# Performance work log

Measured on AMD Instinct MI355X. Metric: run time of the kernel, lower is better.

The kernel has to match this reference:

```python
import jax, jax.numpy as jnp
import numpy as np

N, E, D = 20000, 160000, 128   # nodes, edges, d_model
GH, HC = 4, 128                # TransformerConv heads, per-head channels (= out_channels)
MH = 4                         # temporal MHA heads
MC = D // MH                   # temporal MHA per-head dim
EPS = 1e-5


def layer_norm(x, g, b):
    mu = x.mean(-1, keepdims=True)
    var = ((x - mu) ** 2).mean(-1, keepdims=True)
    return (x - mu) * jax.lax.rsqrt(var + EPS) * g + b


def forward(x, temporal_encoding, gq_w, gq_b, gk_w, gk_b, gv_w, gv_b, gs_w, gs_b,
            mha_wq, mha_bq, mha_wk, mha_bk, mha_wv, mha_bv, mha_wo, mha_bo,
            ffn_w1, ffn_b1, ffn_w2, ffn_b2,
            ln1_g, ln1_b, ln2_g, ln2_b, ln3_g, ln3_b, edge_index):
    src, dst = edge_index[0], edge_index[1]
    n = x.shape[0]
    # --- TransformerConv(in=D, out=D, heads=GH, concat=False, root_weight=True) ---
    q = (x @ gq_w.T + gq_b).reshape(n, GH, HC)
    k = (x @ gk_w.T + gk_b).reshape(n, GH, HC)
    v = (x @ gv_w.T + gv_b).reshape(n, GH, HC)
    # per-edge attention logits: <q_i, k_j> / sqrt(out_channels), message j->i
    alpha = (q[dst] * k[src]).sum(-1) / jnp.sqrt(jnp.asarray(HC, x.dtype))  # [E, GH]
    # numerically-stable segment softmax over incoming edges of each dst node
    m = jax.ops.segment_max(alpha, dst, num_segments=n)                     # [N, GH]
    ex = jnp.exp(alpha - m[dst])
    den = jax.ops.segment_sum(ex, dst, num_segments=n)
    w = ex / den[dst]                                                       # [E, GH]
    agg = jax.ops.segment_sum(w[..., None] * v[src], dst, num_segments=n)  # [N, GH, HC]
    graph_out = agg.mean(1) + (x @ gs_w.T + gs_b)  # concat=False -> head mean; + root skip lin
    x1 = layer_norm(x + graph_out, ln1_g, ln1_b)   # dropout is identity at eval
    # --- temporal MHA: per-node query (len 1) attends to its temporal encoding (kv len 1) ---
    tq = (x1 @ mha_wq.T + mha_bq).reshape(n, MH, MC)
    tk = (temporal_encoding @ mha_wk.T + mha_bk).reshape(n, MH, MC)
    tv = (temporal_encoding @ mha_wv.T + mha_bv).reshape(n, MH, MC)
    scores = (tq * tk).sum(-1, keepdims=True) / jnp.sqrt(jnp.asarray(MC, x.dtype))  # [N, MH, 1]
    attn = jax.nn.softmax(scores, axis=-1)  # exactly ones (single kv position); kept for fidelity
    temp_out = (attn * tv).reshape(n, D) @ mha_wo.T + mha_bo
    x2 = layer_norm(x1 + temp_out, ln2_g, ln2_b)
    # --- FFN ---
    h = jax.nn.relu(x2 @ ffn_w1.T + ffn_b1)
    ffn_out = h @ ffn_w2.T + ffn_b2
    return layer_norm(x2 + ffn_out, ln3_g, ln3_b)


def setup_inputs() -> dict:
    ks = jax.random.split(jax.random.key(0), 16)
    s = 0.05
    def p(i, shape):
        return jax.random.normal(ks[i], shape, jnp.float32) * s
    z = lambda *sh: jnp.zeros(sh, jnp.float32)
    o = lambda *sh: jnp.ones(sh, jnp.float32)
    return {
        "x": p(0, (N, D)),
        "temporal_encoding": p(1, (N, D)),
        "gq_w": p(2, (GH * HC, D)), "gq_b": z(GH * HC),
        "gk_w": p(3, (GH * HC, D)), "gk_b": z(GH * HC),
        "gv_w": p(4, (GH * HC, D)), "gv_b": z(GH * HC),
        "gs_w": p(5, (D, D)), "gs_b": z(D),
        "mha_wq": p(6, (D, D)), "mha_bq": z(D),
        "mha_wk": p(7, (D, D)), "mha_bk": z(D),
        "mha_wv": p(8, (D, D)), "mha_bv": z(D),
        "mha_wo": p(9, (D, D)), "mha_bo": z(D),
        "ffn_w1": p(10, (4 * D, D)), "ffn_b1": z(4 * D),
        "ffn_w2": p(11, (D, 4 * D)), "ffn_b2": z(D),
        "ln1_g": o(D), "ln1_b": z(D),
        "ln2_g": o(D), "ln2_b": z(D),
        "ln3_g": o(D), "ln3_b": z(D),
        "edge_index": jax.random.randint(ks[12], (2, E), 0, N, jnp.int32),
    }


def reference(x, temporal_encoding, gq_w, gq_b, gk_w, gk_b, gv_w, gv_b, gs_w, gs_b,
              mha_wq, mha_bq, mha_wk, mha_bk, mha_wv, mha_bv, mha_wo, mha_bo,
              ffn_w1, ffn_b1, ffn_w2, ffn_b2,
              ln1_g, ln1_b, ln2_g, ln2_b, ln3_g, ln3_b, edge_index):
    return forward(x, temporal_encoding, gq_w, gq_b, gk_w, gk_b, gv_w, gv_b, gs_w, gs_b,
                   mha_wq, mha_bq, mha_wk, mha_bk, mha_wv, mha_bv, mha_wo, mha_bo,
                   ffn_w1, ffn_b1, ffn_w2, ffn_b2,
                   ln1_g, ln1_b, ln2_g, ln2_b, ln3_g, ln3_b, edge_index)
```

## Files before the change

### kernel.cpp

```cpp
#include <hip/hip_runtime.h>

#define NN 20000
#define EE 160000
#define DD 128
#define GHC 512
#define INV_SQRT_HC 0.08838834764831845f

typedef __attribute__((ext_vector_type(8))) short short8;
typedef __attribute__((ext_vector_type(4))) short short4v;
typedef __attribute__((ext_vector_type(4))) float float4v;
typedef __attribute__((ext_vector_type(2))) float float2v;
typedef __attribute__((ext_vector_type(4))) unsigned uint4v;
typedef __attribute__((ext_vector_type(2))) unsigned uint2v;

__device__ inline float bf2f(unsigned short u) {
    union { unsigned u; float f; } x; x.u = ((unsigned)u) << 16; return x.f;
}
__device__ inline unsigned short f2bf(float f) {
    union { float f; unsigned u; } x; x.f = f;
    unsigned u = x.u;
    unsigned r = (u + 0x7fffu + ((u >> 16) & 1u)) >> 16;
    return (unsigned short)r;
}
__device__ inline unsigned cvt_pk_bf16(float a, float b) {
    unsigned d;
    asm("v_cvt_pk_bf16_f32 %0, %1, %2" : "=v"(d) : "v"(a), "v"(b));
    return d;
}

__device__ inline void stage16(const short8* gsrc, short8* ldst) {
    __builtin_amdgcn_global_load_lds(
        (const __attribute__((address_space(1))) void*)gsrc,
        (__attribute__((address_space(3))) void*)ldst, 16, 0, 0);
}

#if defined(__has_builtin)
#if __has_builtin(__builtin_amdgcn_cvt_pk_f32_fp8) && __has_builtin(__builtin_amdgcn_cvt_pk_fp8_f32)
#define HW_FP8 1
#endif
#endif
#ifndef HW_FP8
#define HW_FP8 0
#endif

#if !HW_FP8
__device__ inline unsigned char sw_enc_fp8(float f) {
    if (!(f == f)) return 0x7f;
    unsigned s = (f < 0.f) ? 0x80u : 0u;
    float a = fabsf(f);
    if (a >= 448.f) return (unsigned char)(s | 0x7e);
    if (a < 5.96046448e-8f) return (unsigned char)s;
    int e; frexpf(a, &e);
    int E = e - 1;
    if (E < -6) E = -6;
    float q = ldexpf(rintf(ldexpf(a, 3 - E)), E - 3);
    if (q == 0.f) return (unsigned char)s;
    union { float f; unsigned u; } x; x.f = q;
    int qe = (int)((x.u >> 23) & 0xff) - 127;
    if (qe < -6) {
        unsigned mant = (unsigned)rintf(ldexpf(q, 9));
        return (unsigned char)(s | mant);
    }
    unsigned mant = (x.u >> 20) & 7;
    int ebits = qe + 7;
    if (ebits > 15) { ebits = 15; mant = 6; }
    return (unsigned char)(s | ((unsigned)ebits << 3) | mant);
}
__device__ inline float sw_dec_fp8(unsigned char u) {
    unsigned s = u >> 7, e = (u >> 3) & 15, m = u & 7;
    float v = e ? ldexpf((float)(8 + m), (int)e - 10) : ldexpf((float)m, -9);
    return s ? -v : v;
}
#endif

__device__ inline unsigned fp8_enc4(float a, float b, float c, float d) {
#if HW_FP8
    int r = __builtin_amdgcn_cvt_pk_fp8_f32(a, b, 0, false);
    r = __builtin_amdgcn_cvt_pk_fp8_f32(c, d, r, true);
    return (unsigned)r;
#else
    return (unsigned)sw_enc_fp8(a) | ((unsigned)sw_enc_fp8(b) << 8)
         | ((unsigned)sw_enc_fp8(c) << 16) | ((unsigned)sw_enc_fp8(d) << 24);
#endif
}
__device__ inline float2v fp8_dec2_lo(unsigned w) {
#if HW_FP8
    return __builtin_amdgcn_cvt_pk_f32_fp8((int)w, false);
#else
    float2v r;
    r[0] = sw_dec_fp8((unsigned char)(w & 0xff));
    r[1] = sw_dec_fp8((unsigned char)((w >> 8) & 0xff));
    return r;
#endif
}
__device__ inline float2v fp8_dec2_hi(unsigned w) {
#if HW_FP8
    return __builtin_amdgcn_cvt_pk_f32_fp8((int)w, true);
#else
    float2v r;
    r[0] = sw_dec_fp8((unsigned char)((w >> 16) & 0xff));
    r[1] = sw_dec_fp8((unsigned char)(w >> 24));
    return r;
#endif
}

struct WPack { const void* in[18]; };
__device__ __constant__ const int WSZ[18] = {
    65536, 65536, 65536, 512, 512, 512,
    16384, 128, 65536, 512, 65536, 128,
    128, 128, 128, 128, 128, 128 };

__global__ void prep_kernel(const float* __restrict__ x, const float* __restrict__ te,
                            unsigned short* __restrict__ xcout, WPack p,
                            unsigned short* __restrict__ wcout,
                            const float* __restrict__ wv, const float* __restrict__ bv,
                            const float* __restrict__ wo, const float* __restrict__ bo,
                            unsigned short* __restrict__ wcomb,
                            unsigned short* __restrict__ bcomb,
                            const int* __restrict__ e_dst, int* __restrict__ counts)
{
    const int b = blockIdx.x;
    const int tid = threadIdx.x;
    if (b < 1024) {
        const long n4half = (long)NN * DD / 4;
        short4v* out4 = reinterpret_cast<short4v*>(xcout);
        long i = (long)b * 256 + tid;
        const long stride = 1024L * 256;
        const long tot = 2 * n4half;
        for (; i < tot; i += stride) {
            const float4v* src = (i < n4half)
                ? reinterpret_cast<const float4v*>(x)
                : reinterpret_cast<const float4v*>(te) - n4half;
            float4v v = src[i];
            short4v o;
            o[0] = (short)f2bf(v[0]); o[1] = (short)f2bf(v[1]);
            o[2] = (short)f2bf(v[2]); o[3] = (short)f2bf(v[3]);
            out4[i] = o;
        }
    } else if (b < 1600) {
        const int seg = (b - 1024) >> 5;
        const int rep = (b - 1024) & 31;
        int off = 0;
#pragma unroll
        for (int s = 0; s < 18; ++s) if (s < seg) off += WSZ[s];
        const int n = WSZ[seg];
        const float* q = (const float*)p.in[seg];
        for (int i = rep * 256 + tid; i < n; i += 32 * 256)
            wcout[off + i] = f2bf(q[i]);
    } else if (b < 1664) {
        int e = (b - 1600) * 256 + tid;
        int i = e >> 7, kk = e & 127;
        float s = 0.f;
        for (int j = 0; j < 128; ++j)
            s += wo[i * 128 + j] * wv[j * 128 + kk];
        wcomb[e] = f2bf(s);
        if (b == 1600 && tid < 128) {
            float t = 0.f;
            for (int j = 0; j < 128; ++j) t += wo[tid * 128 + j] * bv[j];
            bcomb[tid] = f2bf(t + bo[tid]);
        }
    } else {
        int e = (b - 1664) * 256 + tid;
        if (e < EE) {
            int d = e_dst[e];
            if (d >= 0 && d < NN) atomicAdd(&counts[d], 1);
        }
    }
}

__global__ __launch_bounds__(256) void gemm3_kernel(
    const unsigned short* __restrict__ A, const unsigned short* __restrict__ W,
    const unsigned short* __restrict__ bias, unsigned short* __restrict__ out,
    unsigned char* __restrict__ kvout, int M, int Nout, int split, int relu,
    int nxg, int ncol)
{
    __shared__ short8 wslab[2048];
    __shared__ __attribute__((aligned(16))) unsigned stile4[4][16][32];
    const int tid  = threadIdx.x;
    const int lane = tid & 63;
    const int wid  = tid >> 6;
    const int quad = lane >> 4;
    const int l15  = lane & 15;

    const int nb  = nxg * ncol;
    const int qq  = nb >> 3, rm = nb & 7;
    const int xcd = blockIdx.x & 7, slot = blockIdx.x >> 3;
    const int c   = (xcd < rm) ? xcd * (qq + 1) + slot
                               : rm * (qq + 1) + (xcd - rm) * qq + slot;
    const int xg = c / ncol;
    const int yg = c - xg * ncol;
    const int colbase0 = yg * 128;
    const int rowg = xg * 256;

    const bool isfp8 = (colbase0 >= split);
    const int kvcol = colbase0 - split;
    const int which = isfp8 ? (kvcol >> 9) : 0;
    const int head  = isfp8 ? ((kvcol & 511) >> 7) : 0;

    const short8* A8 = reinterpret_cast<const short8*>(A);
    const short8* W8 = reinterpret_cast<const short8*>(W);

    short8 a4[4];
    {
        int arow = rowg + wid * 16 + l15;
        if (arow >= M) arow = M - 1;
#pragma unroll
        for (int i = 0; i < 4; ++i) a4[i] = A8[(size_t)arow * 16 + i * 4 + quad];
    }

#pragma unroll
    for (int rep = 0; rep < 8; ++rep) {
        const int fi  = (rep * 4 + wid) & 3;
        const int ft  = rep & 3;
        const int ftt = rep >> 2;
        const int wrow = colbase0 + ftt * 64 + 16 * ft + l15;
        stage16(&W8[(size_t)wrow * 16 + fi * 4 + quad], &wslab[rep * 256 + wid * 64]);
    }

    short4v bs4[2][4];
#pragma unroll
    for (int tt = 0; tt < 2; ++tt)
#pragma unroll
        for (int t = 0; t < 4; ++t)
            bs4[tt][t] = *reinterpret_cast<const short4v*>(
                &bias[colbase0 + tt * 64 + 16 * t + quad * 4]);

    __syncthreads();

    unsigned* fpd = &stile4[wid][0][0];

#pragma unroll
    for (int tg = 0; tg < 4; ++tg) {
        const int rowbase = rowg + tg * 64 + wid * 16;

        short8 a4n[4];
        if (tg < 3) {
            int arow = rowbase + 64 + l15;
            if (arow >= M) arow = M - 1;
#pragma unroll
            for (int i = 0; i < 4; ++i) a4n[i] = A8[(size_t)arow * 16 + i * 4 + quad];
        }

#pragma unroll
        for (int tt = 0; tt < 2; ++tt) {
            float4v acc[4];
#pragma unroll
            for (int t = 0; t < 4; ++t) acc[t] = (float4v){0.f, 0.f, 0.f, 0.f};

#pragma unroll
            for (int i = 0; i < 4; ++i) {
#pragma unroll
                for (int t = 0; t < 4; ++t) {
                    short8 wb = wslab[((tt * 4 + t) * 4 + i) * 64 + lane];
                    acc[t] = __builtin_amdgcn_mfma_f32_16x16x32_bf16(wb, a4[i], acc[t], 0, 0, 0);
                }
            }

            if (!isfp8) {
#pragma unroll
                for (int t = 0; t < 4; ++t) {
                    float v0 = acc[t][0] + bf2f((unsigned short)bs4[tt][t][0]);
                    float v1 = acc[t][1] + bf2f((unsigned short)bs4[tt][t][1]);
                    float v2 = acc[t][2] + bf2f((unsigned short)bs4[tt][t][2]);
                    float v3 = acc[t][3] + bf2f((unsigned short)bs4[tt][t][3]);
                    if (relu) {
                        v0 = fmaxf(v0, 0.f); v1 = fmaxf(v1, 0.f);
                        v2 = fmaxf(v2, 0.f); v3 = fmaxf(v3, 0.f);
                    }
                    uint2v d = { cvt_pk_bf16(v0, v1), cvt_pk_bf16(v2, v3) };
                    const int dc = (8 * t + quad * 2) ^ ((l15 & 7) << 2);
                    *reinterpret_cast<uint2v*>(&stile4[wid][l15][dc]) = d;
                }
                const int rr0 = lane >> 3;
                const int cd  = (lane & 7) * 4;
#pragma unroll
                for (int it = 0; it < 2; ++it) {
                    int rw = rr0 + it * 8;
                    int grow = rowbase + rw;
                    if (grow < M) {
                        const int cs = cd ^ ((rw & 7) << 2);
                        uint4v v = *reinterpret_cast<const uint4v*>(&stile4[wid][rw][cs]);
                        *reinterpret_cast<uint4v*>(&out[(size_t)grow * Nout + colbase0 + tt * 64 + cd * 2]) = v;
                    }
                }
            } else {
#pragma unroll
                for (int t = 0; t < 4; ++t) {
                    float v0 = (acc[t][0] + bf2f((unsigned short)bs4[tt][t][0])) * 256.f;
                    float v1 = (acc[t][1] + bf2f((unsigned short)bs4[tt][t][1])) * 256.f;
                    float v2 = (acc[t][2] + bf2f((unsigned short)bs4[tt][t][2])) * 256.f;
                    float v3 = (acc[t][3] + bf2f((unsigned short)bs4[tt][t][3])) * 256.f;
                    const int dc = (tt * 16 + 4 * t + quad) ^ ((l15 & 7) << 2);
                    fpd[l15 * 32 + dc] = fp8_enc4(v0, v1, v2, v3);
                }
            }
        }

        if (isfp8) {
#pragma unroll
            for (int it = 0; it < 2; ++it) {
                int u = lane + it * 64;
                int row = u >> 3;
                int part = u & 7;
                int grow = rowbase + row;
                if (grow < M) {
                    const int db = row * 32 + ((part * 4) ^ ((row & 7) << 2));
                    uint4v v = *reinterpret_cast<const uint4v*>(&fpd[db]);
                    size_t ro = (size_t)grow * 1024 + (size_t)which * 512
                              + (size_t)head * 128 + (size_t)part * 16;
                    *reinterpret_cast<uint4v*>(kvout + ro) = v;
                }
            }
        }

        if (tg < 3) {
#pragma unroll
            for (int i = 0; i < 4; ++i) a4[i] = a4n[i];
        }
    }
}

__global__ __launch_bounds__(256) void gemm_ln2_kernel(
    const unsigned short* __restrict__ A, const unsigned short* __restrict__ W,
    const unsigned short* __restrict__ bias,
    const float* __restrict__ residf, const float* __restrict__ c,
    const unsigned short* __restrict__ g, const unsigned short* __restrict__ beta,
    float* __restrict__ outf, unsigned short* __restrict__ outb, int M, int K)
{
    __shared__ short8 wslab[2048];
    const int tid  = threadIdx.x;
    const int lane = tid & 63;
    const int wid  = tid >> 6;
    const int quad = lane >> 4;
    const int l15  = lane & 15;
    const int rowbase = blockIdx.x * 64 + wid * 16;

    const int grow = rowbase + l15;
    const int gr = (grow < M) ? grow : M - 1;

    const short8* A8 = reinterpret_cast<const short8*>(A);
    const short8* W8 = reinterpret_cast<const short8*>(W);
    const int k8 = K >> 3;
    const int kchunks = K >> 7;

    float4v acc[2][4];
#pragma unroll
    for (int tt = 0; tt < 2; ++tt)
#pragma unroll
        for (int t = 0; t < 4; ++t) acc[tt][t] = (float4v){0.f, 0.f, 0.f, 0.f};

    for (int cc = 0; cc < kchunks; ++cc) {
        if (cc > 0) __syncthreads();
#pragma unroll
        for (int rep = 0; rep < 8; ++rep) {
            const int fi  = (rep * 4 + wid) & 3;
            const int ft  = rep & 3;
            const int ftt = rep >> 2;
            const int wrow = ftt * 64 + 16 * ft + l15;
            stage16(&W8[(size_t)wrow * k8 + cc * 16 + fi * 4 + quad],
                    &wslab[rep * 256 + wid * 64]);
        }
        short8 a4[4];
#pragma unroll
        for (int i = 0; i < 4; ++i) a4[i] = A8[(size_t)gr * k8 + cc * 16 + i * 4 + quad];
        __syncthreads();
#pragma unroll
        for (int tt = 0; tt < 2; ++tt)
#pragma unroll
            for (int i = 0; i < 4; ++i)
#pragma unroll
                for (int t = 0; t < 4; ++t) {
                    short8 wb = wslab[((tt * 4 + t) * 4 + i) * 64 + lane];
                    acc[tt][t] = __builtin_amdgcn_mfma_f32_16x16x32_bf16(wb, a4[i], acc[tt][t], 0, 0, 0);
                }
    }

    float v[32];
#pragma unroll
    for (int tt = 0; tt < 2; ++tt)
#pragma unroll
        for (int t = 0; t < 4; ++t) {
            const int n0 = tt * 64 + 16 * t + quad * 4;
            short4v bs = *reinterpret_cast<const short4v*>(&bias[n0]);
            float4v rv = *reinterpret_cast<const float4v*>(&residf[(size_t)gr * 128 + n0]);
#pragma unroll
            for (int r = 0; r < 4; ++r)
                v[(tt * 4 + t) * 4 + r] = acc[tt][t][r]
                    + bf2f((unsigned short)bs[r]) + rv[r];
        }
    if (c) {
#pragma unroll
        for (int tt = 0; tt < 2; ++tt)
#pragma unroll
            for (int t = 0; t < 4; ++t) {
                const int n0 = tt * 64 + 16 * t + quad * 4;
                float4v cv = *reinterpret_cast<const float4v*>(&c[(size_t)gr * 128 + n0]);
#pragma unroll
                for (int r = 0; r < 4; ++r) v[(tt * 4 + t) * 4 + r] += cv[r];
            }
    }
    float s = 0.f, sq = 0.f;
#pragma unroll
    for (int i = 0; i < 32; ++i) { s += v[i]; sq += v[i] * v[i]; }
    s  += __shfl_xor(s, 16, 64);  s  += __shfl_xor(s, 32, 64);
    sq += __shfl_xor(sq, 16, 64); sq += __shfl_xor(sq, 32, 64);
    float mu  = s * (1.f / 128.f);
    float var = sq * (1.f / 128.f) - mu * mu;
    float rs  = rsqrtf(fmaxf(var, 0.f) + 1e-5f);

    if (grow < M) {
#pragma unroll
        for (int tt = 0; tt < 2; ++tt)
#pragma unroll
            for (int t = 0; t < 4; ++t) {
                const int n0 = tt * 64 + 16 * t + quad * 4;
                short4v gg = *reinterpret_cast<const short4v*>(&g[n0]);
                short4v bb = *reinterpret_cast<const short4v*>(&beta[n0]);
                float4v ov;
#pragma unroll
                for (int r = 0; r < 4; ++r)
                    ov[r] = (v[(tt * 4 + t) * 4 + r] - mu) * rs
                            * bf2f((unsigned short)gg[r]) + bf2f((unsigned short)bb[r]);
                *reinterpret_cast<float4v*>(&outf[(size_t)grow * 128 + n0]) = ov;
                if (outb) {
                    uint2v d = { cvt_pk_bf16(ov[0], ov[1]), cvt_pk_bf16(ov[2], ov[3]) };
                    *reinterpret_cast<uint2v*>(&outb[(size_t)grow * 128 + n0]) = d;
                }
            }
    }
}

__global__ __launch_bounds__(256) void gemm_ln12_kernel(
    const unsigned short* __restrict__ A1, const unsigned short* __restrict__ W1,
    const unsigned short* __restrict__ b1,
    const float* __restrict__ rx, const float* __restrict__ ragg,
    const unsigned short* __restrict__ g1, const unsigned short* __restrict__ be1,
    const unsigned short* __restrict__ A2, const unsigned short* __restrict__ W2,
    const unsigned short* __restrict__ b2,
    const unsigned short* __restrict__ g2, const unsigned short* __restrict__ be2,
    float* __restrict__ outf, unsigned short* __restrict__ outb, int M)
{
    __shared__ short8 wslab[2048];
    const int tid  = threadIdx.x;
    const int lane = tid & 63;
    const int wid  = tid >> 6;
    const int quad = lane >> 4;
    const int l15  = lane & 15;
    const int rowbase = blockIdx.x * 64 + wid * 16;

    const int grow = rowbase + l15;
    const int gr = (grow < M) ? grow : M - 1;

    const short8* A81 = reinterpret_cast<const short8*>(A1);
    const short8* A82 = reinterpret_cast<const short8*>(A2);
    const short8* W81 = reinterpret_cast<const short8*>(W1);
    const short8* W82 = reinterpret_cast<const short8*>(W2);

#pragma unroll
    for (int rep = 0; rep < 8; ++rep) {
        const int fi  = (rep * 4 + wid) & 3;
        const int ft  = rep & 3;
        const int ftt = rep >> 2;
        const int wrow = ftt * 64 + 16 * ft + l15;
        stage16(&W81[(size_t)wrow * 16 + fi * 4 + quad], &wslab[rep * 256 + wid * 64]);
    }
    short8 a4[4];
#pragma unroll
    for (int i = 0; i < 4; ++i) a4[i] = A81[(size_t)gr * 16 + i * 4 + quad];
    __syncthreads();

    float4v acc1[2][4];
#pragma unroll
    for (int tt = 0; tt < 2; ++tt)
#pragma unroll
        for (int t = 0; t < 4; ++t) acc1[tt][t] = (float4v){0.f, 0.f, 0.f, 0.f};
#pragma unroll
    for (int tt = 0; tt < 2; ++tt)
#pragma unroll
        for (int i = 0; i < 4; ++i)
#pragma unroll
            for (int t = 0; t < 4; ++t) {
                short8 wb = wslab[((tt * 4 + t) * 4 + i) * 64 + lane];
                acc1[tt][t] = __builtin_amdgcn_mfma_f32_16x16x32_bf16(wb, a4[i], acc1[tt][t], 0, 0, 0);
            }
    __syncthreads();

#pragma unroll
    for (int rep = 0; rep < 8; ++rep) {
        const int fi  = (rep * 4 + wid) & 3;
        const int ft  = rep & 3;
        const int ftt = rep >> 2;
        const int wrow = ftt * 64 + 16 * ft + l15;
        stage16(&W82[(size_t)wrow * 16 + fi * 4 + quad], &wslab[rep * 256 + wid * 64]);
    }
    short8 a42[4];
#pragma unroll
    for (int i = 0; i < 4; ++i) a42[i] = A82[(size_t)gr * 16 + i * 4 + quad];

    float x1[32];
    {
        float v[32];
#pragma unroll
        for (int tt = 0; tt < 2; ++tt)
#pragma unroll
            for (int t = 0; t < 4; ++t) {
                const int n0 = tt * 64 + 16 * t + quad * 4;
                short4v bs = *reinterpret_cast<const short4v*>(&b1[n0]);
                float4v rv = *reinterpret_cast<const float4v*>(&rx[(size_t)gr * 128 + n0]);
                float4v cv = *reinterpret_cast<const float4v*>(&ragg[(size_t)gr * 128 + n0]);
#pragma unroll
                for (int r = 0; r < 4; ++r)
                    v[(tt * 4 + t) * 4 + r] = acc1[tt][t][r]
                        + bf2f((unsigned short)bs[r]) + rv[r] + cv[r];
            }
        float s = 0.f, sq = 0.f;
#pragma unroll
        for (int i = 0; i < 32; ++i) { s += v[i]; sq += v[i] * v[i]; }
        s  += __shfl_xor(s, 16, 64);  s  += __shfl_xor(s, 32, 64);
        sq += __shfl_xor(sq, 16, 64); sq += __shfl_xor(sq, 32, 64);
        float mu  = s * (1.f / 128.f);
        float var = sq * (1.f / 128.f) - mu * mu;
        float rs  = rsqrtf(fmaxf(var, 0.f) + 1e-5f);
#pragma unroll
        for (int tt = 0; tt < 2; ++tt)
#pragma unroll
            for (int t = 0; t < 4; ++t) {
                const int n0 = tt * 64 + 16 * t + quad * 4;
                short4v gg = *reinterpret_cast<const short4v*>(&g1[n0]);
                short4v bb = *reinterpret_cast<const short4v*>(&be1[n0]);
#pragma unroll
                for (int r = 0; r < 4; ++r)
                    x1[(tt * 4 + t) * 4 + r] = (v[(tt * 4 + t) * 4 + r] - mu) * rs
                        * bf2f((unsigned short)gg[r]) + bf2f((unsigned short)bb[r]);
            }
    }

    __syncthreads();

    float4v acc2[2][4];
#pragma unroll
    for (int tt = 0; tt < 2; ++tt)
#pragma unroll
        for (int t = 0; t < 4; ++t) acc2[tt][t] = (float4v){0.f, 0.f, 0.f, 0.f};
#pragma unroll
    for (int tt = 0; tt < 2; ++tt)
#pragma unroll
        for (int i = 0; i < 4; ++i)
#pragma unroll
            for (int t = 0; t < 4; ++t) {
                short8 wb = wslab[((tt * 4 + t) * 4 + i) * 64 + lane];
                acc2[tt][t] = __builtin_amdgcn_mfma_f32_16x16x32_bf16(wb, a42[i], acc2[tt][t], 0, 0, 0);
            }

    float v[32];
#pragma unroll
    for (int tt = 0; tt < 2; ++tt)
#pragma unroll
        for (int t = 0; t < 4; ++t) {
            const int n0 = tt * 64 + 16 * t + quad * 4;
            short4v bs = *reinterpret_cast<const short4v*>(&b2[n0]);
#pragma unroll
            for (int r = 0; r < 4; ++r)
                v[(tt * 4 + t) * 4 + r] = acc2[tt][t][r]
                    + bf2f((unsigned short)bs[r]) + x1[(tt * 4 + t) * 4 + r];
        }
    float s = 0.f, sq = 0.f;
#pragma unroll
    for (int i = 0; i < 32; ++i) { s += v[i]; sq += v[i] * v[i]; }
    s  += __shfl_xor(s, 16, 64);  s  += __shfl_xor(s, 32, 64);
    sq += __shfl_xor(sq, 16, 64); sq += __shfl_xor(sq, 32, 64);
    float mu  = s * (1.f / 128.f);
    float var = sq * (1.f / 128.f) - mu * mu;
    float rs  = rsqrtf(fmaxf(var, 0.f) + 1e-5f);

    if (grow < M) {
#pragma unroll
        for (int tt = 0; tt < 2; ++tt)
#pragma unroll
            for (int t = 0; t < 4; ++t) {
                const int n0 = tt * 64 + 16 * t + quad * 4;
                short4v gg = *reinterpret_cast<const short4v*>(&g2[n0]);
                short4v bb = *reinterpret_cast<const short4v*>(&be2[n0]);
                float4v ov;
#pragma unroll
                for (int r = 0; r < 4; ++r)
                    ov[r] = (v[(tt * 4 + t) * 4 + r] - mu) * rs
                            * bf2f((unsigned short)gg[r]) + bf2f((unsigned short)bb[r]);
                *reinterpret_cast<float4v*>(&outf[(size_t)grow * 128 + n0]) = ov;
                uint2v d = { cvt_pk_bf16(ov[0], ov[1]), cvt_pk_bf16(ov[2], ov[3]) };
                *reinterpret_cast<uint2v*>(&outb[(size_t)grow * 128 + n0]) = d;
            }
    }
}

__global__ __launch_bounds__(1024) void scan_kernel(
    const int* __restrict__ counts, int* __restrict__ offsets, int* __restrict__ pos, int n)
{
    __shared__ int wsum[16];
    __shared__ int carry_s;
    const int tid = threadIdx.x;
    const int wid = tid >> 6, lane = tid & 63;
    int vals[20];
#pragma unroll
    for (int cI = 0; cI < 20; ++cI) {
        int i = cI * 1024 + tid;
        vals[cI] = (i < n) ? counts[i] : 0;
    }
    if (tid == 0) carry_s = 0;
    __syncthreads();
#pragma unroll
    for (int cI = 0; cI < 20; ++cI) {
        int i = cI * 1024 + tid;
        int val = vals[cI];
        int x = val;
#pragma unroll
        for (int off = 1; off < 64; off <<= 1) {
            int t = __shfl_up(x, off, 64);
            if (lane >= off) x += t;
        }
        if (lane == 63) wsum[wid] = x;
        __syncthreads();
        if (wid == 0 && lane < 16) {
            int s = wsum[lane];
#pragma unroll
            for (int off = 1; off < 16; off <<= 1) {
                int t = __shfl_up(s, off, 64);
                if (lane >= off) s += t;
            }
            wsum[lane] = s;
        }
        __syncthreads();
        int prefix = (wid > 0 ? wsum[wid - 1] : 0) + carry_s;
        int ex = prefix + x - val;
        if (i < n) { offsets[i] = ex; pos[i] = ex; }
        __syncthreads();
        if (tid == 0) carry_s += wsum[15];
        __syncthreads();
    }
    if (tid == 0) offsets[n] = carry_s;
}

__global__ void scatter_kernel(const int* __restrict__ src, const int* __restrict__ dst,
                               int* __restrict__ pos, int* __restrict__ sorted_src, int E)
{
    int e = blockIdx.x * 256 + threadIdx.x;
    if (e < E) {
        int d = dst[e];
        if (d >= 0 && d < NN) {
            int p = atomicAdd(&pos[d], 1);
            if (p >= 0 && p < E) sorted_src[p] = src[e];
        }
    }
}

__device__ inline void agg_edge(const uint2v& kk, const uint2v& vv,
                                const float* qf, float* acc, float& ssum)
{
    float2v k01 = fp8_dec2_lo(kk[0]);
    float2v k23 = fp8_dec2_hi(kk[0]);
    float2v k45 = fp8_dec2_lo(kk[1]);
    float2v k67 = fp8_dec2_hi(kk[1]);
    float dot = qf[0] * k01[0] + qf[1] * k01[1] + qf[2] * k23[0] + qf[3] * k23[1]
              + qf[4] * k45[0] + qf[5] * k45[1] + qf[6] * k67[0] + qf[7] * k67[1];
    dot += __shfl_xor(dot, 1, 64);
    dot += __shfl_xor(dot, 2, 64);
    dot += __shfl_xor(dot, 4, 64);
    dot += __shfl_xor(dot, 8, 64);
    float pp = __expf(dot);
    ssum += pp;
    float2v v01 = fp8_dec2_lo(vv[0]);
    float2v v23 = fp8_dec2_hi(vv[0]);
    float2v v45 = fp8_dec2_lo(vv[1]);
    float2v v67 = fp8_dec2_hi(vv[1]);
    acc[0] += pp * v01[0]; acc[1] += pp * v01[1];
    acc[2] += pp * v23[0]; acc[3] += pp * v23[1];
    acc[4] += pp * v45[0]; acc[5] += pp * v45[1];
    acc[6] += pp * v67[0]; acc[7] += pp * v67[1];
}

__global__ __launch_bounds__(256) void agg_kernel(
    const unsigned short* __restrict__ q, const unsigned char* __restrict__ kvb,
    const int* __restrict__ offsets, const int* __restrict__ srcs,
    float* __restrict__ aggb)
{
    __shared__ float sacc[4][64][9];
    __shared__ float sssum[4][64];
    const int tid  = threadIdx.x;
    const int wid  = tid >> 6;
    const int lane = tid & 63;
    const int node = blockIdx.x * 2 + (wid >> 1);
    const int half = wid & 1;

    const short8* q8 = reinterpret_cast<const short8*>(q);
    const int fidx = (lane >> 4) * 16 + (lane & 15);
    const int koff = fidx * 8;

    short8 qv = q8[(size_t)node * 64 + fidx];
    float qf[8];
#pragma unroll
    for (int i = 0; i < 8; ++i)
        qf[i] = bf2f((unsigned short)qv[i]) * (INV_SQRT_HC / 256.f);

    int beg = offsets[node], end = offsets[node + 1];
    if (beg < 0) beg = 0;
    if (end > EE) end = EE;
    float ssum = 0.f;
    float acc[8];
#pragma unroll
    for (int i = 0; i < 8; ++i) acc[i] = 0.f;

    const int start = beg + half;
    int nce = (end > start) ? ((end - start + 1) >> 1) : 0;
    int ncap = (nce > 64) ? 64 : nce;

    int sv = 0;
    if (lane < ncap) {
        int s = srcs[start + 2 * lane];
        if (s < 0) s = 0;
        if (s >= NN) s = NN - 1;
        sv = s;
    }
    for (int base = 0; base < ncap; base += 4) {
        const int rem = ncap - base;
        uint2v k0{}, v0{}, k1{}, v1{}, k2{}, v2{}, k3{}, v3{};
        {
            int s = __shfl(sv, base, 64);
            const unsigned char* p = kvb + (size_t)s * 1024 + koff;
            k0 = *reinterpret_cast<const uint2v*>(p);
            v0 = *reinterpret_cast<const uint2v*>(p + 512);
        }
        if (rem > 1) {
            int s = __shfl(sv, base + 1, 64);
            const unsigned char* p = kvb + (size_t)s * 1024 + koff;
            k1 = *reinterpret_cast<const uint2v*>(p);
            v1 = *reinterpret_cast<const uint2v*>(p + 512);
        }
        if (rem > 2) {
            int s = __shfl(sv, base + 2, 64);
            const unsigned char* p = kvb + (size_t)s * 1024 + koff;
            k2 = *reinterpret_cast<const uint2v*>(p);
            v2 = *reinterpret_cast<const uint2v*>(p + 512);
        }
        if (rem > 3) {
            int s = __shfl(sv, base + 3, 64);
            const unsigned char* p = kvb + (size_t)s * 1024 + koff;
            k3 = *reinterpret_cast<const uint2v*>(p);
            v3 = *reinterpret_cast<const uint2v*>(p + 512);
        }
        agg_edge(k0, v0, qf, acc, ssum);
        if (rem > 1) agg_edge(k1, v1, qf, acc, ssum);
        if (rem > 2) agg_edge(k2, v2, qf, acc, ssum);
        if (rem > 3) agg_edge(k3, v3, qf, acc, ssum);
    }
    for (int j = start + 128; j < end; j += 2) {
        int s = srcs[j];
        if (s < 0) s = 0;
        if (s >= NN) s = NN - 1;
        uint2v kc = *reinterpret_cast<const uint2v*>(kvb + (size_t)s * 1024 + koff);
        uint2v vc = *reinterpret_cast<const uint2v*>(kvb + (size_t)s * 1024 + 512 + koff);
        agg_edge(kc, vc, qf, acc, ssum);
    }

#pragma unroll
    for (int i = 0; i < 8; ++i) sacc[wid][lane][i] = acc[i];
    sssum[wid][lane] = ssum;
    __syncthreads();
    if (half == 0) {
#pragma unroll
        for (int i = 0; i < 8; ++i) acc[i] += sacc[wid ^ 1][lane][i];
        ssum += sssum[wid ^ 1][lane];

        float inv = (ssum > 0.f) ? 1.f / (256.f * ssum) : 0.f;
#pragma unroll
        for (int i = 0; i < 8; ++i) acc[i] *= inv;
#pragma unroll
        for (int i = 0; i < 8; ++i) {
            acc[i] += __shfl_xor(acc[i], 16, 64);
            acc[i] += __shfl_xor(acc[i], 32, 64);
            acc[i] *= 0.25f;
        }
        if (lane < 16) {
            float4v* o = reinterpret_cast<float4v*>(aggb + (size_t)node * 128 + lane * 8);
            o[0] = (float4v){acc[0], acc[1], acc[2], acc[3]};
            o[1] = (float4v){acc[4], acc[5], acc[6], acc[7]};
        }
    }
}

extern "C" void kernel_launch(void* const* d_in, const int* in_sizes, int n_in,
                              void* d_out, int out_size, void* d_ws, size_t ws_size,
                              hipStream_t stream)
{
    const int* edge_index = (const int*)d_in[28];
    const int* e_src = edge_index;
    const int* e_dst = edge_index + EE;

    if (n_in < 29 || in_sizes[0] != NN * DD || in_sizes[28] != 2 * EE || out_size != NN * DD)
        return;

    const size_t SZ_OFF  = (size_t)(NN + 16) * 4;
    const size_t SZ_CNT  = (size_t)NN * 4;
    const size_t SZ_SS   = (size_t)EE * 4;
    const size_t SZ_SM   = (size_t)NN * DD * 2;
    const size_t SZ_F32  = (size_t)NN * DD * 4;
    const size_t SZ_Q    = (size_t)NN * 512 * 2;
    const size_t SZ_KV   = (size_t)NN * 1024;
    const size_t SZ_HB   = (size_t)NN * GHC * 2;
    const size_t WC_ELE  = 347136;
    const size_t SZ_WC   = WC_ELE * 2;
    const size_t SZ_WCB  = 16384 * 2 + 256;
    const size_t REQUIRED = SZ_OFF + 2 * SZ_CNT + SZ_SS + 2 * SZ_SM + SZ_WC + SZ_WCB
                          + SZ_Q + SZ_KV + 3 * SZ_F32 + SZ_SM + SZ_HB;

    if (ws_size < REQUIRED) return;

    char* w = (char*)d_ws;
    int* offsets = (int*)w;        w += SZ_OFF;
    int* counts  = (int*)w;        w += SZ_CNT;
    int* pos     = (int*)w;        w += SZ_CNT;
    int* sorted_src = (int*)w;     w += SZ_SS;
    unsigned short* xc   = (unsigned short*)w; w += SZ_SM;
    unsigned short* tec  = (unsigned short*)w; w += SZ_SM;
    unsigned short* wc   = (unsigned short*)w; w += SZ_WC;
    unsigned short* wcomb = (unsigned short*)w; w += 16384 * 2;
    unsigned short* bcomb = (unsigned short*)w; w += 256;
    unsigned short* qb   = (unsigned short*)w; w += SZ_Q;
    unsigned char*  kvb  = (unsigned char*)w;  w += SZ_KV;
    float*          aggb = (float*)w;          w += SZ_F32;
    float*          x1f  = (float*)w;          w += SZ_F32;
    float*          x2f  = (float*)w;          w += SZ_F32;
    unsigned short* x2b  = (unsigned short*)w; w += SZ_SM;
    unsigned short* hbuf = (unsigned short*)w; w += SZ_HB;
    (void)x1f;

    unsigned short* cw = wc;
    unsigned short* qkv_w = cw; cw += 3 * 65536;
    unsigned short* qkv_b = cw; cw += 3 * 512;
    unsigned short* gs_w  = cw; cw += 16384;  unsigned short* gs_b  = cw; cw += 128;
    unsigned short* ffn_w1 = cw; cw += 65536; unsigned short* ffn_b1 = cw; cw += 512;
    unsigned short* ffn_w2 = cw; cw += 65536; unsigned short* ffn_b2 = cw; cw += 128;
    unsigned short* ln1_g = cw; cw += 128;    unsigned short* ln1_b = cw; cw += 128;
    unsigned short* ln2_g = cw; cw += 128;    unsigned short* ln2_b = cw; cw += 128;
    unsigned short* ln3_g = cw; cw += 128;    unsigned short* ln3_b = cw; cw += 128;

    const int EB = (EE + 255) / 256;
    const dim3 blk(256);
    const int MB = (NN + 63) / 64;
    const int MB2 = (NN + 255) / 256;

    WPack pack;
    const int live_idx[18] = {2,4,6, 3,5,7, 8,9, 18,19, 20,21, 22,23,24,25,26,27};
    for (int i = 0; i < 18; ++i) pack.in[i] = d_in[live_idx[i]];

    (void)hipMemsetAsync(counts, 0, SZ_CNT, stream);
    prep_kernel<<<1664 + EB, blk, 0, stream>>>((const float*)d_in[0], (const float*)d_in[1],
                                               xc, pack, wc,
                                               (const float*)d_in[14], (const float*)d_in[15],
                                               (const float*)d_in[16], (const float*)d_in[17],
                                               wcomb, bcomb, e_dst, counts);

    scan_kernel<<<1, 1024, 0, stream>>>(counts, offsets, pos, NN);
    scatter_kernel<<<EB, blk, 0, stream>>>(e_src, e_dst, pos, sorted_src, EE);

    gemm3_kernel<<<dim3(MB2 * 12), blk, 0, stream>>>(xc, qkv_w, qkv_b, qb, kvb,
                                                     NN, 512, 512, 0, MB2, 12);
    agg_kernel<<<NN / 2, blk, 0, stream>>>(qb, kvb, offsets, sorted_src, aggb);
    gemm_ln12_kernel<<<MB, blk, 0, stream>>>(xc, gs_w, gs_b,
                                             (const float*)d_in[0], aggb,
                                             ln1_g, ln1_b,
                                             tec, wcomb, bcomb,
                                             ln2_g, ln2_b, x2f, x2b, NN);
    gemm3_kernel<<<dim3(MB2 * 4), blk, 0, stream>>>(x2b, ffn_w1, ffn_b1, hbuf, nullptr,
                                                    NN, 512, 99999, 1, MB2, 4);
    gemm_ln2_kernel<<<MB, blk, 0, stream>>>(hbuf, ffn_w2, ffn_b2, x2f, nullptr,
                                            ln3_g, ln3_b, (float*)d_out, nullptr, NN, GHC);
}
```

Measured before the change: 259.8 us.

## Fuse LN1/LN2 GEMMs and full FFN into a single tail kernel

Merges the root-skip GEMM + LN1, temporal GEMM + LN2, FFN up-projection with ReLU, and FFN down-projection + LN3 into one kernel per 64-row tile. The 512-wide hidden activation is produced and consumed in 128-column chunks through a swizzled LDS tile, so it never goes to global memory. The x2 float/bf16 intermediates also stay on chip. This removes two launches and the global round trips of x2 and the hidden buffer. In exchange it adds LDS use, register pressure, more barriers, and only 313 blocks of parallelism for the FFN work instead of a wider grid.

```diff
diff --git a/kernel.cpp b/kernel.cpp
--- a/kernel.cpp
+++ b/kernel.cpp
@@ -320,50 +320,252 @@
     }
 }
 
-__global__ __launch_bounds__(256) void gemm_ln2_kernel(
-    const unsigned short* __restrict__ A, const unsigned short* __restrict__ W,
-    const unsigned short* __restrict__ bias,
-    const float* __restrict__ residf, const float* __restrict__ c,
-    const unsigned short* __restrict__ g, const unsigned short* __restrict__ beta,
-    float* __restrict__ outf, unsigned short* __restrict__ outb, int M, int K)
+__global__ __launch_bounds__(256) void tail_kernel(
+    const unsigned short* __restrict__ A1, const unsigned short* __restrict__ W1g,
+    const unsigned short* __restrict__ b1g,
+    const unsigned short* __restrict__ A2, const unsigned short* __restrict__ W2g,
+    const unsigned short* __restrict__ b2g,
+    const float* __restrict__ rx, const float* __restrict__ ragg,
+    const unsigned short* __restrict__ g1, const unsigned short* __restrict__ be1,
+    const unsigned short* __restrict__ g2, const unsigned short* __restrict__ be2,
+    const unsigned short* __restrict__ fw1, const unsigned short* __restrict__ fb1,
+    const unsigned short* __restrict__ fw2, const unsigned short* __restrict__ fb2,
+    const unsigned short* __restrict__ g3, const unsigned short* __restrict__ be3,
+    float* __restrict__ outf, int M)
 {
     __shared__ short8 wslab[2048];
+    __shared__ __attribute__((aligned(16))) unsigned short htile[64 * 128];
     const int tid  = threadIdx.x;
     const int lane = tid & 63;
     const int wid  = tid >> 6;
     const int quad = lane >> 4;
     const int l15  = lane & 15;
     const int rowbase = blockIdx.x * 64 + wid * 16;
-
     const int grow = rowbase + l15;
     const int gr = (grow < M) ? grow : M - 1;
-
-    const short8* A8 = reinterpret_cast<const short8*>(A);
-    const short8* W8 = reinterpret_cast<const short8*>(W);
-    const int k8 = K >> 3;
-    const int kchunks = K >> 7;
-
-    float4v acc[2][4];
+    const int hrow = wid * 16 + l15;
+    char* hb = reinterpret_cast<char*>(htile);
+
+    const short8* A81 = reinterpret_cast<const short8*>(A1);
+    const short8* A82 = reinterpret_cast<const short8*>(A2);
+    const short8* W81 = reinterpret_cast<const short8*>(W1g);
+    const short8* W82 = reinterpret_cast<const short8*>(W2g);
+    const short8* F18 = reinterpret_cast<const short8*>(fw1);
+    const short8* F28 = reinterpret_cast<const short8*>(fw2);
+
+#pragma unroll
+    for (int rep = 0; rep < 8; ++rep) {
+        const int fi  = (rep * 4 + wid) & 3;
+        const int ft  = rep & 3;
+        const int ftt = rep >> 2;
+        const int wrow = ftt * 64 + 16 * ft + l15;
+        stage16(&W81[(size_t)wrow * 16 + fi * 4 + quad], &wslab[rep * 256 + wid * 64]);
+    }
+    short8 a4[4];
+#pragma unroll
+    for (int i = 0; i < 4; ++i) a4[i] = A81[(size_t)gr * 16 + i * 4 + quad];
+    __syncthreads();
+
+    float4v acc1[2][4];
 #pragma unroll
     for (int tt = 0; tt < 2; ++tt)
 #pragma unroll
-        for (int t = 0; t < 4; ++t) acc[tt][t] = (float4v){0.f, 0.f, 0.f, 0.f};
-
-    for (int cc = 0; cc < kchunks; ++cc) {
-        if (cc > 0) __syncthreads();
+        for (int t = 0; t < 4; ++t) acc1[tt][t] = (float4v){0.f, 0.f, 0.f, 0.f};
+#pragma unroll
+    for (int tt = 0; tt < 2; ++tt)
+#pragma unroll
+        for (int i = 0; i < 4; ++i)
+#pragma unroll
+            for (int t = 0; t < 4; ++t) {
+                short8 wb = wslab[((tt * 4 + t) * 4 + i) * 64 + lane];
+                acc1[tt][t] = __builtin_amdgcn_mfma_f32_16x16x32_bf16(wb, a4[i], acc1[tt][t], 0, 0, 0);
+            }
+    __syncthreads();
+
+#pragma unroll
+    for (int rep = 0; rep < 8; ++rep) {
+        const int fi  = (rep * 4 + wid) & 3;
+        const int ft  = rep & 3;
+        const int ftt = rep >> 2;
+        const int wrow = ftt * 64 + 16 * ft + l15;
+        stage16(&W82[(size_t)wrow * 16 + fi * 4 + quad], &wslab[rep * 256 + wid * 64]);
+    }
+    short8 a42[4];
+#pragma unroll
+    for (int i = 0; i < 4; ++i) a42[i] = A82[(size_t)gr * 16 + i * 4 + quad];
+
+    float x1[32];
+    {
+        float v[32];
+#pragma unroll
+        for (int tt = 0; tt < 2; ++tt)
+#pragma unroll
+            for (int t = 0; t < 4; ++t) {
+                const int n0 = tt * 64 + 16 * t + quad * 4;
+                short4v bs = *reinterpret_cast<const short4v*>(&b1g[n0]);
+                float4v rv = *reinterpret_cast<const float4v*>(&rx[(size_t)gr * 128 + n0]);
+                float4v cv = *reinterpret_cast<const float4v*>(&ragg[(size_t)gr * 128 + n0]);
+#pragma unroll
+                for (int r = 0; r < 4; ++r)
+                    v[(tt * 4 + t) * 4 + r] = acc1[tt][t][r]
+                        + bf2f((unsigned short)bs[r]) + rv[r] + cv[r];
+            }
+        float s = 0.f, sq = 0.f;
+#pragma unroll
+        for (int i = 0; i < 32; ++i) { s += v[i]; sq += v[i] * v[i]; }
+        s  += __shfl_xor(s, 16, 64);  s  += __shfl_xor(s, 32, 64);
+        sq += __shfl_xor(sq, 16, 64); sq += __shfl_xor(sq, 32, 64);
+        float mu  = s * (1.f / 128.f);
+        float var = sq * (1.f / 128.f) - mu * mu;
+        float rs  = rsqrtf(fmaxf(var, 0.f) + 1e-5f);
+#pragma unroll
+        for (int tt = 0; tt < 2; ++tt)
+#pragma unroll
+            for (int t = 0; t < 4; ++t) {
+                const int n0 = tt * 64 + 16 * t + quad * 4;
+                short4v gg = *reinterpret_cast<const short4v*>(&g1[n0]);
+                short4v bb = *reinterpret_cast<const short4v*>(&be1[n0]);
+#pragma unroll
+                for (int r = 0; r < 4; ++r)
+                    x1[(tt * 4 + t) * 4 + r] = (v[(tt * 4 + t) * 4 + r] - mu) * rs
+                        * bf2f((unsigned short)gg[r]) + bf2f((unsigned short)bb[r]);
+            }
+    }
+
+    __syncthreads();
+
+    float4v acc2[2][4];
+#pragma unroll
+    for (int tt = 0; tt < 2; ++tt)
+#pragma unroll
+        for (int t = 0; t < 4; ++t) acc2[tt][t] = (float4v){0.f, 0.f, 0.f, 0.f};
+#pragma unroll
+    for (int tt = 0; tt < 2; ++tt)
+#pragma unroll
+        for (int i = 0; i < 4; ++i)
+#pragma unroll
+            for (int t = 0; t < 4; ++t) {
+                short8 wb = wslab[((tt * 4 + t) * 4 + i) * 64 + lane];
+                acc2[tt][t] = __builtin_amdgcn_mfma_f32_16x16x32_bf16(wb, a42[i], acc2[tt][t], 0, 0, 0);
+            }
+
+    float x2[32];
+    {
+        float v[32];
+#pragma unroll
+        for (int tt = 0; tt < 2; ++tt)
+#pragma unroll
+            for (int t = 0; t < 4; ++t) {
+                const int n0 = tt * 64 + 16 * t + quad * 4;
+                short4v bs = *reinterpret_cast<const short4v*>(&b2g[n0]);
+#pragma unroll
+                for (int r = 0; r < 4; ++r)
+                    v[(tt * 4 + t) * 4 + r] = acc2[tt][t][r]
+                        + bf2f((unsigned short)bs[r]) + x1[(tt * 4 + t) * 4 + r];
+            }
+        float s = 0.f, sq = 0.f;
+#pragma unroll
+        for (int i = 0; i < 32; ++i) { s += v[i]; sq += v[i] * v[i]; }
+        s  += __shfl_xor(s, 16, 64);  s  += __shfl_xor(s, 32, 64);
+        sq += __shfl_xor(sq, 16, 64); sq += __shfl_xor(sq, 32, 64);
+        float mu  = s * (1.f / 128.f);
+        float var = sq * (1.f / 128.f) - mu * mu;
+        float rs  = rsqrtf(fmaxf(var, 0.f) + 1e-5f);
+#pragma unroll
+        for (int tt = 0; tt < 2; ++tt)
+#pragma unroll
+            for (int t = 0; t < 4; ++t) {
+                const int n0 = tt * 64 + 16 * t + quad * 4;
+                short4v gg = *reinterpret_cast<const short4v*>(&g2[n0]);
+                short4v bb = *reinterpret_cast<const short4v*>(&be2[n0]);
+#pragma unroll
+                for (int r = 0; r < 4; ++r)
+                    x2[(tt * 4 + t) * 4 + r] = (v[(tt * 4 + t) * 4 + r] - mu) * rs
+                        * bf2f((unsigned short)gg[r]) + bf2f((unsigned short)bb[r]);
+            }
+    }
+
+#pragma unroll
+    for (int tt = 0; tt < 2; ++tt)
+#pragma unroll
+        for (int t = 0; t < 4; ++t) {
+            const int n0 = tt * 64 + 16 * t + quad * 4;
+            const int idx = (tt * 4 + t) * 4;
+            uint2v d = { cvt_pk_bf16(x2[idx], x2[idx + 1]),
+                         cvt_pk_bf16(x2[idx + 2], x2[idx + 3]) };
+            *reinterpret_cast<uint2v*>(
+                hb + ((hrow * 256 + n0 * 2) ^ ((hrow & 7) << 4))) = d;
+        }
+    short8 af[4];
+#pragma unroll
+    for (int i = 0; i < 4; ++i)
+        af[i] = *reinterpret_cast<const short8*>(
+            hb + ((hrow * 256 + (i * 32 + quad * 8) * 2) ^ ((hrow & 7) << 4)));
+
+    float4v accf[2][4];
+#pragma unroll
+    for (int tt = 0; tt < 2; ++tt)
+#pragma unroll
+        for (int t = 0; t < 4; ++t) accf[tt][t] = (float4v){0.f, 0.f, 0.f, 0.f};
+
+    for (int cc = 0; cc < 4; ++cc) {
+        __syncthreads();
+#pragma unroll
+        for (int rep = 0; rep < 8; ++rep) {
+            const int fi  = (rep * 4 + wid) & 3;
+            const int ft  = rep & 3;
+            const int ftt = rep >> 2;
+            const int wrow = cc * 128 + ftt * 64 + 16 * ft + l15;
+            stage16(&F18[(size_t)wrow * 16 + fi * 4 + quad], &wslab[rep * 256 + wid * 64]);
+        }
+        __syncthreads();
+
+        float4v au[2][4];
+#pragma unroll
+        for (int tt = 0; tt < 2; ++tt)
+#pragma unroll
+            for (int t = 0; t < 4; ++t) au[tt][t] = (float4v){0.f, 0.f, 0.f, 0.f};
+#pragma unroll
+        for (int tt = 0; tt < 2; ++tt)
+#pragma unroll
+            for (int i = 0; i < 4; ++i)
+#pragma unroll
+                for (int t = 0; t < 4; ++t) {
+                    short8 wb = wslab[((tt * 4 + t) * 4 + i) * 64 + lane];
+                    au[tt][t] = __builtin_amdgcn_mfma_f32_16x16x32_bf16(wb, af[i], au[tt][t], 0, 0, 0);
+                }
+#pragma unroll
+        for (int tt = 0; tt < 2; ++tt)
+#pragma unroll
+            for (int t = 0; t < 4; ++t) {
+                const int n0 = tt * 64 + 16 * t + quad * 4;
+                short4v bs = *reinterpret_cast<const short4v*>(&fb1[cc * 128 + n0]);
+                float v0 = fmaxf(au[tt][t][0] + bf2f((unsigned short)bs[0]), 0.f);
+                float v1 = fmaxf(au[tt][t][1] + bf2f((unsigned short)bs[1]), 0.f);
+                float v2 = fmaxf(au[tt][t][2] + bf2f((unsigned short)bs[2]), 0.f);
+                float v3 = fmaxf(au[tt][t][3] + bf2f((unsigned short)bs[3]), 0.f);
+                uint2v d = { cvt_pk_bf16(v0, v1), cvt_pk_bf16(v2, v3) };
+                *reinterpret_cast<uint2v*>(
+                    hb + ((hrow * 256 + n0 * 2) ^ ((hrow & 7) << 4))) = d;
+            }
+
+        __syncthreads();
 #pragma unroll
         for (int rep = 0; rep < 8; ++rep) {
             const int fi  = (rep * 4 + wid) & 3;
             const int ft  = rep & 3;
             const int ftt = rep >> 2;
             const int wrow = ftt * 64 + 16 * ft + l15;
-            stage16(&W8[(size_t)wrow * k8 + cc * 16 + fi * 4 + quad],
+            stage16(&F28[(size_t)wrow * 64 + cc * 16 + fi * 4 + quad],
                     &wslab[rep * 256 + wid * 64]);
         }
-        short8 a4[4];
-#pragma unroll
-        for (int i = 0; i < 4; ++i) a4[i] = A8[(size_t)gr * k8 + cc * 16 + i * 4 + quad];
         __syncthreads();
+
+        short8 h4[4];
+#pragma unroll
+        for (int i = 0; i < 4; ++i)
+            h4[i] = *reinterpret_cast<const short8*>(
+                hb + ((hrow * 256 + (i * 32 + quad * 8) * 2) ^ ((hrow & 7) << 4)));
 #pragma unroll
         for (int tt = 0; tt < 2; ++tt)
 #pragma unroll
@@ -371,7 +573,7 @@
 #pragma unroll
                 for (int t = 0; t < 4; ++t) {
                     short8 wb = wslab[((tt * 4 + t) * 4 + i) * 64 + lane];
-                    acc[tt][t] = __builtin_amdgcn_mfma_f32_16x16x32_bf16(wb, a4[i], acc[tt][t], 0, 0, 0);
+                    accf[tt][t] = __builtin_amdgcn_mfma_f32_16x16x32_bf16(wb, h4[i], accf[tt][t], 0, 0, 0);
                 }
     }
 
@@ -381,24 +583,12 @@
 #pragma unroll
         for (int t = 0; t < 4; ++t) {
             const int n0 = tt * 64 + 16 * t + quad * 4;
-            short4v bs = *reinterpret_cast<const short4v*>(&bias[n0]);
-            float4v rv = *reinterpret_cast<const float4v*>(&residf[(size_t)gr * 128 + n0]);
+            short4v bs = *reinterpret_cast<const short4v*>(&fb2[n0]);
 #pragma unroll
             for (int r = 0; r < 4; ++r)
-                v[(tt * 4 + t) * 4 + r] = acc[tt][t][r]
-                    + bf2f((unsigned short)bs[r]) + rv[r];
-        }
-    if (c) {
-#pragma unroll
-        for (int tt = 0; tt < 2; ++tt)
-#pragma unroll
-            for (int t = 0; t < 4; ++t) {
-                const int n0 = tt * 64 + 16 * t + quad * 4;
-                float4v cv = *reinterpret_cast<const float4v*>(&c[(size_t)gr * 128 + n0]);
-#pragma unroll
-                for (int r = 0; r < 4; ++r) v[(tt * 4 + t) * 4 + r] += cv[r];
-            }
-    }
+                v[(tt * 4 + t) * 4 + r] = accf[tt][t][r]
+                    + bf2f((unsigned short)bs[r]) + x2[(tt * 4 + t) * 4 + r];
+        }
     float s = 0.f, sq = 0.f;
 #pragma unroll
     for (int i = 0; i < 32; ++i) { s += v[i]; sq += v[i] * v[i]; }
@@ -414,181 +604,14 @@
 #pragma unroll
             for (int t = 0; t < 4; ++t) {
                 const int n0 = tt * 64 + 16 * t + quad * 4;
-                short4v gg = *reinterpret_cast<const short4v*>(&g[n0]);
-                short4v bb = *reinterpret_cast<const short4v*>(&beta[n0]);
+                short4v gg = *reinterpret_cast<const short4v*>(&g3[n0]);
+                short4v bb = *reinterpret_cast<const short4v*>(&be3[n0]);
                 float4v ov;
 #pragma unroll
                 for (int r = 0; r < 4; ++r)
                     ov[r] = (v[(tt * 4 + t) * 4 + r] - mu) * rs
                             * bf2f((unsigned short)gg[r]) + bf2f((unsigned short)bb[r]);
                 *reinterpret_cast<float4v*>(&outf[(size_t)grow * 128 + n0]) = ov;
-                if (outb) {
-                    uint2v d = { cvt_pk_bf16(ov[0], ov[1]), cvt_pk_bf16(ov[2], ov[3]) };
-                    *reinterpret_cast<uint2v*>(&outb[(size_t)grow * 128 + n0]) = d;
-                }
-            }
-    }
-}
-
-__global__ __launch_bounds__(256) void gemm_ln12_kernel(
-    const unsigned short* __restrict__ A1, const unsigned short* __restrict__ W1,
-    const unsigned short* __restrict__ b1,
-    const float* __restrict__ rx, const float* __restrict__ ragg,
-    const unsigned short* __restrict__ g1, const unsigned short* __restrict__ be1,
-    const unsigned short* __restrict__ A2, const unsigned short* __restrict__ W2,
-    const unsigned short* __restrict__ b2,
-    const unsigned short* __restrict__ g2, const unsigned short* __restrict__ be2,
-    float* __restrict__ outf, unsigned short* __restrict__ outb, int M)
-{
-    __shared__ short8 wslab[2048];
-    const int tid  = threadIdx.x;
-    const int lane = tid & 63;
-    const int wid  = tid >> 6;
-    const int quad = lane >> 4;
-    const int l15  = lane & 15;
-    const int rowbase = blockIdx.x * 64 + wid * 16;
-
-    const int grow = rowbase + l15;
-    const int gr = (grow < M) ? grow : M - 1;
-
-    const short8* A81 = reinterpret_cast<const short8*>(A1);
-    const short8* A82 = reinterpret_cast<const short8*>(A2);
-    const short8* W81 = reinterpret_cast<const short8*>(W1);
-    const short8* W82 = reinterpret_cast<const short8*>(W2);
-
-#pragma unroll
-    for (int rep = 0; rep < 8; ++rep) {
-        const int fi  = (rep * 4 + wid) & 3;
-        const int ft  = rep & 3;
-        const int ftt = rep >> 2;
-        const int wrow = ftt * 64 + 16 * ft + l15;
-        stage16(&W81[(size_t)wrow * 16 + fi * 4 + quad], &wslab[rep * 256 + wid * 64]);
-    }
-    short8 a4[4];
-#pragma unroll
-    for (int i = 0; i < 4; ++i) a4[i] = A81[(size_t)gr * 16 + i * 4 + quad];
-    __syncthreads();
-
-    float4v acc1[2][4];
-#pragma unroll
-    for (int tt = 0; tt < 2; ++tt)
-#pragma unroll
-        for (int t = 0; t < 4; ++t) acc1[tt][t] = (float4v){0.f, 0.f, 0.f, 0.f};
-#pragma unroll
-    for (int tt = 0; tt < 2; ++tt)
-#pragma unroll
-        for (int i = 0; i < 4; ++i)
-#pragma unroll
-            for (int t = 0; t < 4; ++t) {
-                short8 wb = wslab[((tt * 4 + t) * 4 + i) * 64 + lane];
-                acc1[tt][t] = __builtin_amdgcn_mfma_f32_16x16x32_bf16(wb, a4[i], acc1[tt][t], 0, 0, 0);
-            }
-    __syncthreads();
-
-#pragma unroll
-    for (int rep = 0; rep < 8; ++rep) {
-        const int fi  = (rep * 4 + wid) & 3;
-        const int ft  = rep & 3;
-        const int ftt = rep >> 2;
-        const int wrow = ftt * 64 + 16 * ft + l15;
-        stage16(&W82[(size_t)wrow * 16 + fi * 4 + quad], &wslab[rep * 256 + wid * 64]);
-    }
-    short8 a42[4];
-#pragma unroll
-    for (int i = 0; i < 4; ++i) a42[i] = A82[(size_t)gr * 16 + i * 4 + quad];
-
-    float x1[32];
-    {
-        float v[32];
-#pragma unroll
-        for (int tt = 0; tt < 2; ++tt)
-#pragma unroll
-            for (int t = 0; t < 4; ++t) {
-                const int n0 = tt * 64 + 16 * t + quad * 4;
-                short4v bs = *reinterpret_cast<const short4v*>(&b1[n0]);
-                float4v rv = *reinterpret_cast<const float4v*>(&rx[(size_t)gr * 128 + n0]);
-                float4v cv = *reinterpret_cast<const float4v*>(&ragg[(size_t)gr * 128 + n0]);
-#pragma unroll
-                for (int r = 0; r < 4; ++r)
-                    v[(tt * 4 + t) * 4 + r] = acc1[tt][t][r]
-                        + bf2f((unsigned short)bs[r]) + rv[r] + cv[r];
-            }
-        float s = 0.f, sq = 0.f;
-#pragma unroll
-        for (int i = 0; i < 32; ++i) { s += v[i]; sq += v[i] * v[i]; }
-        s  += __shfl_xor(s, 16, 64);  s  += __shfl_xor(s, 32, 64);
-        sq += __shfl_xor(sq, 16, 64); sq += __shfl_xor(sq, 32, 64);
-        float mu  = s * (1.f / 128.f);
-        float var = sq * (1.f / 128.f) - mu * mu;
-        float rs  = rsqrtf(fmaxf(var, 0.f) + 1e-5f);
-#pragma unroll
-        for (int tt = 0; tt < 2; ++tt)
-#pragma unroll
-            for (int t = 0; t < 4; ++t) {
-                const int n0 = tt * 64 + 16 * t + quad * 4;
-                short4v gg = *reinterpret_cast<const short4v*>(&g1[n0]);
-                short4v bb = *reinterpret_cast<const short4v*>(&be1[n0]);
-#pragma unroll
-                for (int r = 0; r < 4; ++r)
-                    x1[(tt * 4 + t) * 4 + r] = (v[(tt * 4 + t) * 4 + r] - mu) * rs
-                        * bf2f((unsigned short)gg[r]) + bf2f((unsigned short)bb[r]);
-            }
-    }
-
-    __syncthreads();
-
-    float4v acc2[2][4];
-#pragma unroll
-    for (int tt = 0; tt < 2; ++tt)
-#pragma unroll
-        for (int t = 0; t < 4; ++t) acc2[tt][t] = (float4v){0.f, 0.f, 0.f, 0.f};
-#pragma unroll
-    for (int tt = 0; tt < 2; ++tt)
-#pragma unroll
-        for (int i = 0; i < 4; ++i)
-#pragma unroll
-            for (int t = 0; t < 4; ++t) {
-                short8 wb = wslab[((tt * 4 + t) * 4 + i) * 64 + lane];
-                acc2[tt][t] = __builtin_amdgcn_mfma_f32_16x16x32_bf16(wb, a42[i], acc2[tt][t], 0, 0, 0);
-            }
-
-    float v[32];
-#pragma unroll
-    for (int tt = 0; tt < 2; ++tt)
-#pragma unroll
-        for (int t = 0; t < 4; ++t) {
-            const int n0 = tt * 64 + 16 * t + quad * 4;
-            short4v bs = *reinterpret_cast<const short4v*>(&b2[n0]);
-#pragma unroll
-            for (int r = 0; r < 4; ++r)
-                v[(tt * 4 + t) * 4 + r] = acc2[tt][t][r]
-                    + bf2f((unsigned short)bs[r]) + x1[(tt * 4 + t) * 4 + r];
-        }
-    float s = 0.f, sq = 0.f;
-#pragma unroll
-    for (int i = 0; i < 32; ++i) { s += v[i]; sq += v[i] * v[i]; }
-    s  += __shfl_xor(s, 16, 64);  s  += __shfl_xor(s, 32, 64);
-    sq += __shfl_xor(sq, 16, 64); sq += __shfl_xor(sq, 32, 64);
-    float mu  = s * (1.f / 128.f);
-    float var = sq * (1.f / 128.f) - mu * mu;
-    float rs  = rsqrtf(fmaxf(var, 0.f) + 1e-5f);
-
-    if (grow < M) {
-#pragma unroll
-        for (int tt = 0; tt < 2; ++tt)
-#pragma unroll
-            for (int t = 0; t < 4; ++t) {
-                const int n0 = tt * 64 + 16 * t + quad * 4;
-                short4v gg = *reinterpret_cast<const short4v*>(&g2[n0]);
-                short4v bb = *reinterpret_cast<const short4v*>(&be2[n0]);
-                float4v ov;
-#pragma unroll
-                for (int r = 0; r < 4; ++r)
-                    ov[r] = (v[(tt * 4 + t) * 4 + r] - mu) * rs
-                            * bf2f((unsigned short)gg[r]) + bf2f((unsigned short)bb[r]);
-                *reinterpret_cast<float4v*>(&outf[(size_t)grow * 128 + n0]) = ov;
-                uint2v d = { cvt_pk_bf16(ov[0], ov[1]), cvt_pk_bf16(ov[2], ov[3]) };
-                *reinterpret_cast<uint2v*>(&outb[(size_t)grow * 128 + n0]) = d;
             }
     }
 }
@@ -831,7 +854,7 @@
     float*          x2f  = (float*)w;          w += SZ_F32;
     unsigned short* x2b  = (unsigned short*)w; w += SZ_SM;
     unsigned short* hbuf = (unsigned short*)w; w += SZ_HB;
-    (void)x1f;
+    (void)x1f; (void)x2f; (void)x2b; (void)hbuf;
 
     unsigned short* cw = wc;
     unsigned short* qkv_w = cw; cw += 3 * 65536;
@@ -865,13 +888,11 @@
     gemm3_kernel<<<dim3(MB2 * 12), blk, 0, stream>>>(xc, qkv_w, qkv_b, qb, kvb,
                                                      NN, 512, 512, 0, MB2, 12);
     agg_kernel<<<NN / 2, blk, 0, stream>>>(qb, kvb, offsets, sorted_src, aggb);
-    gemm_ln12_kernel<<<MB, blk, 0, stream>>>(xc, gs_w, gs_b,
-                                             (const float*)d_in[0], aggb,
-                                             ln1_g, ln1_b,
-                                             tec, wcomb, bcomb,
-                                             ln2_g, ln2_b, x2f, x2b, NN);
-    gemm3_kernel<<<dim3(MB2 * 4), blk, 0, stream>>>(x2b, ffn_w1, ffn_b1, hbuf, nullptr,
-                                                    NN, 512, 99999, 1, MB2, 4);
-    gemm_ln2_kernel<<<MB, blk, 0, stream>>>(hbuf, ffn_w2, ffn_b2, x2f, nullptr,
-                                            ln3_g, ln3_b, (float*)d_out, nullptr, NN, GHC);
-}
+
+    tail_kernel<<<MB, blk, 0, stream>>>(xc, gs_w, gs_b,
+                                        tec, wcomb, bcomb,
+                                        (const float*)d_in[0], aggb,
+                                        ln1_g, ln1_b, ln2_g, ln2_b,
+                                        ffn_w1, ffn_b1, ffn_w2, ffn_b2,
+                                        ln3_g, ln3_b, (float*)d_out, NN);
+}
```

Measured after the change: 251.4 us. 3.2% less time.
